# Optimization experiments

Measured on AMD Instinct MI355X. Metric: run time of the kernel, lower is better.

Reference implementation:

```python
import jax, jax.numpy as jnp
import numpy as np

D = 128
N_A = 50000
N_B = 50000
E = 600000
EPS = 1e-5

def setup_inputs() -> dict:
    key = jax.random.key(0)
    ks = jax.random.split(key, 16)
    s = 1.0 / np.sqrt(D)
    inp = {
        "x_A": jax.random.normal(ks[0], (N_A, D), jnp.float32),
        "x_B": jax.random.normal(ks[1], (N_B, D), jnp.float32),
        "ei_aa": jax.random.randint(ks[2], (2, E), 0, N_A),
        "ei_ba": jnp.stack([jax.random.randint(ks[3], (E,), 0, N_B),
                             jax.random.randint(ks[4], (E,), 0, N_A)]),
        "ei_ab": jnp.stack([jax.random.randint(ks[5], (E,), 0, N_A),
                             jax.random.randint(ks[6], (E,), 0, N_B)]),
        # SAGEConv params per edge type: W_l (neighbor), W_r (root), bias
        "W_l_aa": jax.random.uniform(ks[7], (D, D), jnp.float32, -s, s),
        "W_r_aa": jax.random.uniform(ks[8], (D, D), jnp.float32, -s, s),
        "b_aa": jnp.zeros((D,), jnp.float32),
        "W_l_ba": jax.random.uniform(ks[9], (D, D), jnp.float32, -s, s),
        "W_r_ba": jax.random.uniform(ks[10], (D, D), jnp.float32, -s, s),
        "b_ba": jnp.zeros((D,), jnp.float32),
        "W_l_ab": jax.random.uniform(ks[11], (D, D), jnp.float32, -s, s),
        "W_r_ab": jax.random.uniform(ks[12], (D, D), jnp.float32, -s, s),
        "b_ab": jnp.zeros((D,), jnp.float32),
        "gamma": jnp.ones((D,), jnp.float32),
        "beta": jnp.zeros((D,), jnp.float32),
    }
    return inp

def _sage(x_src, x_dst, ei, W_l, W_r, b, n_dst):
    # mean aggregation of gathered neighbor features (0 for isolated nodes, like PyG)
    msgs = x_src[ei[0]]                                            # [E, D]
    ssum = jax.ops.segment_sum(msgs, ei[1], num_segments=n_dst)    # [n_dst, D]
    cnt = jax.ops.segment_sum(jnp.ones((ei.shape[1], 1), x_src.dtype), ei[1], num_segments=n_dst)
    mean = ssum / jnp.maximum(cnt, 1.0)
    return mean @ W_l.T + x_dst @ W_r.T + b

def _layernorm(x, gamma, beta):
    mu = jnp.mean(x, axis=-1, keepdims=True)
    var = jnp.mean(jnp.square(x - mu), axis=-1, keepdims=True)
    return (x - mu) * jax.lax.rsqrt(var + EPS) * gamma + beta

def reference(x_A, x_B, ei_aa, ei_ba, ei_ab,
              W_l_aa, W_r_aa, b_aa, W_l_ba, W_r_ba, b_ba,
              W_l_ab, W_r_ab, b_ab, gamma, beta):
    # HeteroConv(aggr='sum'): sum conv outputs per destination node type
    out_A = (_sage(x_A, x_A, ei_aa, W_l_aa, W_r_aa, b_aa, N_A)
             + _sage(x_B, x_A, ei_ba, W_l_ba, W_r_ba, b_ba, N_A))
    out_B = _sage(x_A, x_B, ei_ab, W_l_ab, W_r_ab, b_ab, N_B)
    out_A = jax.nn.relu(_layernorm(out_A, gamma, beta))
    out_B = jax.nn.relu(_layernorm(out_B, gamma, beta))
    return out_A, out_B
```

## Files before the change

### kernel.cpp

```cpp
#include <hip/hip_runtime.h>

#define NNODE 50000
#define NEDGE 600000
#define NDST 150000
#define NEALL 1800000
#define BSZ 147
#define NBKT 1021
#define EPB 8192
#define P5B 220
#define PREPB 81
#define ECAP 3072

typedef __attribute__((ext_vector_type(8))) __bf16 bf16x8;
typedef __attribute__((ext_vector_type(4))) float f32x4;
typedef __attribute__((ext_vector_type(4))) unsigned int u32x4;

__device__ int dtype_of(const void* gamma) {
    unsigned int g = *(const unsigned int*)gamma;
    if (g == 0x3F803F80u) return 0;
    if (g == 0x3C003C00u) return 1;
    return 2;
}

__device__ float bf2f(unsigned short u) {
    unsigned int x = ((unsigned int)u) << 16;
    float f;
    __builtin_memcpy(&f, &x, 4);
    return f;
}

__device__ float bflo(unsigned int w) {
    unsigned int x = w << 16;
    float f;
    __builtin_memcpy(&f, &x, 4);
    return f;
}
__device__ float bfhi(unsigned int w) {
    unsigned int x = w & 0xFFFF0000u;
    float f;
    __builtin_memcpy(&f, &x, 4);
    return f;
}

__device__ unsigned short f2bf(float f) {
    unsigned int x;
    __builtin_memcpy(&x, &f, 4);
    unsigned int r = (x + 0x7FFFu + ((x >> 16) & 1u)) >> 16;
    return (unsigned short)r;
}

__device__ float ldf(const void* p, int i, int dt) {
    if (dt == 0) return bf2f(((const unsigned short*)p)[i]);
    if (dt == 1) return (float)(((const _Float16*)p)[i]);
    return ((const float*)p)[i];
}

__device__ void stf(void* p, int i, int dt, float v) {
    if (dt == 0) ((unsigned short*)p)[i] = f2bf(v);
    else if (dt == 1) ((_Float16*)p)[i] = (_Float16)v;
    else ((float*)p)[i] = v;
}

__device__ void edge4(const int* ei_aa, const int* ei_ba, const int* ei_ab,
                      int e, int4* d4, int4* s4) {
    const int* dbase;
    const int* sbase;
    int add;
    if (e < NEDGE) { sbase = ei_aa + e; dbase = ei_aa + NEDGE + e; add = 0; }
    else if (e < 2 * NEDGE) {
        int ee = e - NEDGE;
        sbase = ei_ba + ee; dbase = ei_ba + NEDGE + ee; add = 50000;
    } else {
        int ee = e - 2 * NEDGE;
        sbase = ei_ab + ee; dbase = ei_ab + NEDGE + ee; add = 100000;
    }
    int4 d = *(const int4*)dbase;
    d.x += add; d.y += add; d.z += add; d.w += add;
    *d4 = d;
    *s4 = *(const int4*)sbase;
}

__device__ void prep_body(int idx, const void* Wl_aa, const void* Wr_aa,
                          const void* b_aa, const void* Wl_ba, const void* Wr_ba,
                          const void* b_ba, const void* Wl_ab, const void* Wr_ab,
                          const void* b_ab, unsigned short* WA, unsigned short* WB,
                          float* biasA, float* biasB, int dt) {
    if (idx < 49152) {
        int n = idx / 384;
        int k = idx % 384;
        float v;
        if (k < 128) v = ldf(Wl_aa, n * 128 + k, dt);
        else if (k < 256) v = ldf(Wl_ba, n * 128 + k - 128, dt);
        else v = ldf(Wr_aa, n * 128 + k - 256, dt) + ldf(Wr_ba, n * 128 + k - 256, dt);
        WA[idx] = f2bf(v);
    } else if (idx < 49152 + 32768) {
        int i = idx - 49152;
        int n = i / 256;
        int k = i % 256;
        float v;
        if (k < 128) v = ldf(Wl_ab, n * 128 + k, dt);
        else v = ldf(Wr_ab, n * 128 + k - 128, dt);
        WB[i] = f2bf(v);
    } else if (idx < 49152 + 32768 + 128) {
        int j = idx - (49152 + 32768);
        biasA[j] = ldf(b_aa, j, dt) + ldf(b_ba, j, dt);
    } else if (idx < 49152 + 32768 + 256) {
        int j = idx - (49152 + 32768 + 128);
        biasB[j] = ldf(b_ab, j, dt);
    }
}

__global__ __launch_bounds__(1024) void p5_sort(
    const int* ei_aa, const int* ei_ba, const int* ei_ab,
    unsigned int* blkBuf, int* bbCnt, int* ibOfs,
    const void* Wl_aa, const void* Wr_aa, const void* b_aa,
    const void* Wl_ba, const void* Wr_ba, const void* b_ba,
    const void* Wl_ab, const void* Wr_ab, const void* b_ab,
    unsigned short* WA, unsigned short* WB,
    float* biasA, float* biasB, const void* gam) {
    int t = threadIdx.x;
    if (blockIdx.x >= P5B) {
        int dt = dtype_of(gam);
        int idx = (blockIdx.x - P5B) * 1024 + t;
        prep_body(idx, Wl_aa, Wr_aa, b_aa, Wl_ba, Wr_ba, b_ba,
                  Wl_ab, Wr_ab, b_ab, WA, WB, biasA, biasB, dt);
        return;
    }
    __shared__ int cnt[NBKT];
    __shared__ int ls[1024];
    __shared__ unsigned int buf[EPB];
    int4 dreg[2], sreg[2];
    bool val[2];
    int e0 = blockIdx.x * EPB + t * 8;
#pragma unroll
    for (int u = 0; u < 2; ++u) {
        int e = e0 + u * 4;
        val[u] = e < NEALL;
        if (val[u]) edge4(ei_aa, ei_ba, ei_ab, e, &dreg[u], &sreg[u]);
    }
    if (t < NBKT) cnt[t] = 0;
    __syncthreads();
#pragma unroll
    for (int u = 0; u < 2; ++u) {
        if (val[u]) {
            atomicAdd(&cnt[dreg[u].x / BSZ], 1);
            atomicAdd(&cnt[dreg[u].y / BSZ], 1);
            atomicAdd(&cnt[dreg[u].z / BSZ], 1);
            atomicAdd(&cnt[dreg[u].w / BSZ], 1);
        }
    }
    __syncthreads();
    int v = (t < NBKT) ? cnt[t] : 0;
    ls[t] = v;
    __syncthreads();
    for (int o = 1; o < 1024; o <<= 1) {
        int add = (t >= o) ? ls[t - o] : 0;
        __syncthreads();
        ls[t] += add;
        __syncthreads();
    }
    if (t < NBKT) {
        int excl = ls[t] - v;
        bbCnt[blockIdx.x * NBKT + t] = v;
        ibOfs[blockIdx.x * NBKT + t] = excl;
        cnt[t] = excl;
    }
    __syncthreads();
#pragma unroll
    for (int u = 0; u < 2; ++u) {
        if (val[u]) {
            int dv[4] = {dreg[u].x, dreg[u].y, dreg[u].z, dreg[u].w};
            int sv[4] = {sreg[u].x, sreg[u].y, sreg[u].z, sreg[u].w};
#pragma unroll
            for (int w = 0; w < 4; ++w) {
                int bkt = dv[w] / BSZ;
                int dl = dv[w] - bkt * BSZ;
                int r = atomicAdd(&cnt[bkt], 1);
                buf[r] = ((unsigned int)dl << 16) | (unsigned int)sv[w];
            }
        }
    }
    __syncthreads();
    unsigned int* dst = blkBuf + blockIdx.x * EPB;
#pragma unroll
    for (int u = 0; u < 2; ++u) {
        int idx = t * 8 + u * 4;
        __builtin_nontemporal_store(*(const u32x4*)&buf[idx], (u32x4*)&dst[idx]);
    }
}

__global__ __launch_bounds__(512, 8) void p6g_kernel(
    const unsigned int* blkBuf, const int* bbCnt, const int* ibOfs,
    const void* x_A, const void* x_B,
    unsigned short* mean1, unsigned short* mean2, unsigned short* mean3,
    const void* gam) {
    __shared__ int rp[256];
    __shared__ int runSrc[P5B];
    __shared__ unsigned int ebuf[ECAP];
    __shared__ unsigned short ebuf2[ECAP];
    __shared__ int rowLds[BSZ + 1];
    __shared__ int h[BSZ];
    __shared__ int cur[BSZ];
    __shared__ int sc[256];
    int t = threadIdx.x;
    int j = blockIdx.x;
    int dt = dtype_of(gam);
    int wave = t >> 6;
    int lane = t & 63;

    if (t < 256) {
        int c = (t < P5B) ? bbCnt[t * NBKT + j] : 0;
        rp[t] = c;
        if (t < P5B) runSrc[t] = t * EPB + ibOfs[t * NBKT + j];
    }
    __syncthreads();
    for (int o = 1; o < 256; o <<= 1) {
        int add = (t < 256 && t >= o) ? rp[t - o] : 0;
        __syncthreads();
        if (t < 256) rp[t] += add;
        __syncthreads();
    }
    int tot = rp[P5B - 1];
    bool staged = tot <= ECAP;

    if (staged) {
        for (int r = wave; r < P5B; r += 8) {
            int base = r ? rp[r - 1] : 0;
            int n = rp[r] - base;
            int gs = runSrc[r];
            for (int k = lane; k < n; k += 64)
                ebuf[base + k] = __builtin_nontemporal_load(&blkBuf[gs + k]);
        }
    }
    if (t < BSZ) h[t] = 0;
    __syncthreads();
    if (staged) {
        for (int i = t; i < tot; i += 512)
            atomicAdd(&h[(int)(ebuf[i] >> 16)], 1);
    } else {
        for (int r = wave; r < P5B; r += 8) {
            int base = r ? rp[r - 1] : 0;
            int n = rp[r] - base;
            int gs = runSrc[r];
            for (int k = lane; k < n; k += 64)
                atomicAdd(&h[(int)(blkBuf[gs + k] >> 16)], 1);
        }
    }
    __syncthreads();
    if (t < 256) sc[t] = (t < BSZ) ? h[t] : 0;
    __syncthreads();
    for (int o = 1; o < 256; o <<= 1) {
        int add = (t < 256 && t >= o) ? sc[t - o] : 0;
        __syncthreads();
        if (t < 256) sc[t] += add;
        __syncthreads();
    }
    if (t < BSZ) {
        int excl = sc[t] - h[t];
        rowLds[t] = excl;
        cur[t] = excl;
    }
    if (t == 0) rowLds[BSZ] = tot;
    __syncthreads();
    if (staged) {
        for (int i = t; i < tot; i += 512) {
            unsigned int w = ebuf[i];
            int pos = atomicAdd(&cur[(int)(w >> 16)], 1);
            ebuf2[pos] = (unsigned short)(w & 0xFFFFu);
        }
    }
    __syncthreads();

    int sub = lane >> 4;
    int col = lane & 15;
    for (int dl = wave; dl < BSZ; dl += 8) {
        int d = j * BSZ + dl;
        if (d >= NDST) break;
        const void* x;
        unsigned short* mean;
        int node;
        if (d < 50000) { x = x_A; mean = mean1; node = d; }
        else if (d < 100000) { x = x_B; mean = mean2; node = d - 50000; }
        else { x = x_A; mean = mean3; node = d - 100000; }

        if (!staged) {
            float b0 = 0.f, b1 = 0.f;
            int deg = 0;
            for (int r = 0; r < P5B; ++r) {
                int base = r ? rp[r - 1] : 0;
                int n = rp[r] - base;
                int gs = runSrc[r];
                for (int k = 0; k < n; ++k) {
                    unsigned int w = blkBuf[gs + k];
                    if ((int)(w >> 16) == dl) {
                        int src = (int)(w & 0xFFFFu);
                        if (dt == 0) {
                            unsigned int vv = ((const unsigned int*)x)[src * 64 + lane];
                            b0 += bflo(vv);
                            b1 += bfhi(vv);
                        } else {
                            b0 += ldf(x, src * 128 + 2 * lane, dt);
                            b1 += ldf(x, src * 128 + 2 * lane + 1, dt);
                        }
                        ++deg;
                    }
                }
            }
            float inv = deg ? 1.0f / (float)deg : 0.0f;
            ((unsigned int*)mean)[node * 64 + lane] =
                (unsigned int)f2bf(b0 * inv) | ((unsigned int)f2bf(b1 * inv) << 16);
            continue;
        }

        int beg = rowLds[dl];
        int end = rowLds[dl + 1];

        if (dt == 0) {
            const u32x4* xq = (const u32x4*)x;
            float a[8];
#pragma unroll
            for (int q = 0; q < 8; ++q) a[q] = 0.0f;
            for (int i = beg; i < end; i += 16) {
                int e0 = i + sub;
                int e1 = i + 4 + sub;
                int e2 = i + 8 + sub;
                int e3 = i + 12 + sub;
                bool p0 = e0 < end;
                bool p1 = e1 < end;
                bool p2 = e2 < end;
                bool p3 = e3 < end;
                int s0 = ebuf2[p0 ? e0 : beg];
                int s1 = ebuf2[p1 ? e1 : beg];
                int s2 = ebuf2[p2 ? e2 : beg];
                int s3 = ebuf2[p3 ? e3 : beg];
                u32x4 w0 = xq[s0 * 16 + col];
                u32x4 w1 = xq[s1 * 16 + col];
                u32x4 w2 = xq[s2 * 16 + col];
                u32x4 w3 = xq[s3 * 16 + col];
                if (!p0) w0 = u32x4{0u, 0u, 0u, 0u};
                if (!p1) w1 = u32x4{0u, 0u, 0u, 0u};
                if (!p2) w2 = u32x4{0u, 0u, 0u, 0u};
                if (!p3) w3 = u32x4{0u, 0u, 0u, 0u};
                a[0] += (bflo(w0.x) + bflo(w1.x)) + (bflo(w2.x) + bflo(w3.x));
                a[1] += (bfhi(w0.x) + bfhi(w1.x)) + (bfhi(w2.x) + bfhi(w3.x));
                a[2] += (bflo(w0.y) + bflo(w1.y)) + (bflo(w2.y) + bflo(w3.y));
                a[3] += (bfhi(w0.y) + bfhi(w1.y)) + (bfhi(w2.y) + bfhi(w3.y));
                a[4] += (bflo(w0.z) + bflo(w1.z)) + (bflo(w2.z) + bflo(w3.z));
                a[5] += (bfhi(w0.z) + bfhi(w1.z)) + (bfhi(w2.z) + bfhi(w3.z));
                a[6] += (bflo(w0.w) + bflo(w1.w)) + (bflo(w2.w) + bflo(w3.w));
                a[7] += (bfhi(w0.w) + bfhi(w1.w)) + (bfhi(w2.w) + bfhi(w3.w));
            }
#pragma unroll
            for (int q = 0; q < 8; ++q) {
                a[q] += __shfl_xor(a[q], 16);
                a[q] += __shfl_xor(a[q], 32);
            }
            float inv = (end > beg) ? 1.0f / (float)(end - beg) : 0.0f;
            if (lane < 16) {
                u32x4 o;
                o.x = (unsigned int)f2bf(a[0] * inv) | ((unsigned int)f2bf(a[1] * inv) << 16);
                o.y = (unsigned int)f2bf(a[2] * inv) | ((unsigned int)f2bf(a[3] * inv) << 16);
                o.z = (unsigned int)f2bf(a[4] * inv) | ((unsigned int)f2bf(a[5] * inv) << 16);
                o.w = (unsigned int)f2bf(a[6] * inv) | ((unsigned int)f2bf(a[7] * inv) << 16);
                __builtin_nontemporal_store(o, (u32x4*)mean + node * 16 + lane);
            }
        } else {
            float b0 = 0.f, b1 = 0.f;
            for (int i = beg; i < end; ++i) {
                int src = ebuf2[i];
                b0 += ldf(x, src * 128 + 2 * lane, dt);
                b1 += ldf(x, src * 128 + 2 * lane + 1, dt);
            }
            float inv = (end > beg) ? 1.0f / (float)(end - beg) : 0.0f;
            ((unsigned int*)mean)[node * 64 + lane] =
                (unsigned int)f2bf(b0 * inv) | ((unsigned int)f2bf(b1 * inv) << 16);
        }
    }
}

__device__ bf16x8 pack8(const float* f) {
    unsigned short u[8];
    for (int j = 0; j < 8; ++j) u[j] = f2bf(f[j]);
    bf16x8 r;
    __builtin_memcpy(&r, u, 16);
    return r;
}

template <int KTOT>
__device__ bf16x8 loadA(const unsigned short* mean1, const unsigned short* mean2,
                        const void* x, int r, int k, int dt) {
    if (k < 128) {
        return *(const bf16x8*)(mean1 + r * 128 + k);
    }
    if (KTOT == 384 && k < 256) {
        return *(const bf16x8*)(mean2 + r * 128 + (k - 128));
    }
    int kx = k - (KTOT - 128);
    if (dt == 0) {
        return *(const bf16x8*)((const unsigned short*)x + r * 128 + kx);
    }
    float f[8];
    for (int j = 0; j < 8; ++j) f[j] = ldf(x, r * 128 + kx + j, dt);
    return pack8(f);
}

template <int KTOT>
__device__ void gemm_body(int bx, const unsigned short* mean1,
                          const unsigned short* mean2, const void* x,
                          const unsigned short* Wu, const float* bias,
                          const void* gam, const void* bet, void* out,
                          int rowOff, int dt) {
    int lane = threadIdx.x & 63;
    int wave = threadIdx.x >> 6;
    int q16 = lane >> 4;
    int l16 = lane & 15;
    int mBase = (bx * 4 + wave) * 32;

    int r0 = mBase + l16;
    int r1 = mBase + 16 + l16;
    if (r0 > NNODE - 1) r0 = NNODE - 1;
    if (r1 > NNODE - 1) r1 = NNODE - 1;

    f32x4 acc[2][8];
    for (int rt = 0; rt < 2; ++rt)
        for (int tt = 0; tt < 8; ++tt) acc[rt][tt] = f32x4{0.f, 0.f, 0.f, 0.f};

    const int NCH = KTOT / 32;
    for (int ck = 0; ck < NCH; ++ck) {
        int k = ck * 32 + q16 * 8;
        bf16x8 a0 = loadA<KTOT>(mean1, mean2, x, r0, k, dt);
        bf16x8 a1 = loadA<KTOT>(mean1, mean2, x, r1, k, dt);
#pragma unroll
        for (int tt = 0; tt < 8; ++tt) {
            int n = tt * 16 + l16;
            bf16x8 b = *(const bf16x8*)(Wu + n * KTOT + k);
            acc[0][tt] = __builtin_amdgcn_mfma_f32_16x16x32_bf16(a0, b, acc[0][tt], 0, 0, 0);
            acc[1][tt] = __builtin_amdgcn_mfma_f32_16x16x32_bf16(a1, b, acc[1][tt], 0, 0, 0);
        }
    }

    float g[8], be[8], bs[8];
    for (int tt = 0; tt < 8; ++tt) {
        int j = tt * 16 + l16;
        g[tt] = ldf(gam, j, dt);
        be[tt] = ldf(bet, j, dt);
        bs[tt] = bias[j];
    }

    for (int rt = 0; rt < 2; ++rt) {
        for (int q = 0; q < 4; ++q) {
            int row = mBase + rt * 16 + q16 * 4 + q;
            float v[8];
            float s = 0.f, ss = 0.f;
            for (int tt = 0; tt < 8; ++tt) {
                v[tt] = acc[rt][tt][q] + bs[tt];
                s += v[tt];
                ss += v[tt] * v[tt];
            }
            for (int off = 1; off <= 8; off <<= 1) {
                s += __shfl_xor(s, off);
                ss += __shfl_xor(ss, off);
            }
            float m = s * (1.0f / 128.0f);
            float var = ss * (1.0f / 128.0f) - m * m;
            float rstd = rsqrtf(var + 1e-5f);
            if (row < NNODE) {
                for (int tt = 0; tt < 8; ++tt) {
                    float o = (v[tt] - m) * rstd * g[tt] + be[tt];
                    if (o < 0.0f) o = 0.0f;
                    stf(out, (rowOff + row) * 128 + tt * 16 + l16, dt, o);
                }
            }
        }
    }
}

__global__ __launch_bounds__(256) void gemm_ln_all(
    const unsigned short* mean1, const unsigned short* mean2,
    const unsigned short* mean3, const void* x_A, const void* x_B,
    const unsigned short* WA, const unsigned short* WB,
    const float* bA, const float* bB,
    const void* gam, const void* bet, void* out) {
    int dt = dtype_of(gam);
    if (blockIdx.x < 391)
        gemm_body<384>(blockIdx.x, mean1, mean2, x_A, WA, bA, gam, bet, out, 0, dt);
    else
        gemm_body<256>(blockIdx.x - 391, mean3, nullptr, x_B, WB, bB, gam, bet, out,
                       NNODE, dt);
}

extern "C" void kernel_launch(void* const* d_in, const int* in_sizes, int n_in,
                              void* d_out, int out_size, void* d_ws, size_t ws_size,
                              hipStream_t stream) {
    const void* x_A = d_in[0];
    const void* x_B = d_in[1];
    const int* ei_aa = (const int*)d_in[2];
    const int* ei_ba = (const int*)d_in[3];
    const int* ei_ab = (const int*)d_in[4];
    const void* W_l_aa = d_in[5];
    const void* W_r_aa = d_in[6];
    const void* b_aa = d_in[7];
    const void* W_l_ba = d_in[8];
    const void* W_r_ba = d_in[9];
    const void* b_ba = d_in[10];
    const void* W_l_ab = d_in[11];
    const void* W_r_ab = d_in[12];
    const void* b_ab = d_in[13];
    const void* gam = d_in[14];
    const void* bet = d_in[15];

    int* bbCnt = (int*)d_ws;
    int* ibOfs = bbCnt + P5B * NBKT;
    unsigned int* blkBuf = (unsigned int*)(ibOfs + P5B * NBKT);
    unsigned short* mean1 = (unsigned short*)(blkBuf + P5B * EPB);
    unsigned short* mean2 = mean1 + 6400000;
    unsigned short* mean3 = mean2 + 6400000;
    unsigned short* WA = mean3 + 6400000;
    unsigned short* WB = WA + 49152;
    float* bA = (float*)(WB + 32768);
    float* bB = bA + 128;

    p5_sort<<<P5B + PREPB, 1024, 0, stream>>>(
        ei_aa, ei_ba, ei_ab, blkBuf, bbCnt, ibOfs,
        W_l_aa, W_r_aa, b_aa, W_l_ba, W_r_ba, b_ba,
        W_l_ab, W_r_ab, b_ab, WA, WB, bA, bB, gam);

    p6g_kernel<<<NBKT, 512, 0, stream>>>(blkBuf, bbCnt, ibOfs, x_A, x_B,
                                         mean1, mean2, mean3, gam);

    gemm_ln_all<<<782, 256, 0, stream>>>(mean1, mean2, mean3, x_A, x_B,
                                         WA, WB, bA, bB, gam, bet, d_out);
}
```

Before: 370.9 us.

## Fuse mean aggregation with GEMM+LayerNorm, keeping means in swizzled LDS

Merges the aggregation kernel and the GEMM+LayerNorm kernel into one. Buckets now hold 48 A-nodes, with both of their incoming edge types interleaved, or 96 B-nodes, so each block can compute the full output rows for its nodes. The bf16 means are written to XOR-swizzled shared memory instead of three global mean buffers, which removes a global write/read round trip and a kernel launch. In exchange each block runs the GEMM with only 8 waves and reads weights per block from global/L2. It also adds LDS atomics for the row statistics and cuts the staged edge capacity, so more buckets may fall onto the slow unstaged path.

Result: slower. 537.4 us (+44.9%).

```diff
diff --git a/kernel.cpp b/kernel.cpp
--- a/kernel.cpp
+++ b/kernel.cpp
@@ -4,12 +4,12 @@
 #define NEDGE 600000
 #define NDST 150000
 #define NEALL 1800000
-#define BSZ 147
-#define NBKT 1021
+#define ABKT 1042
+#define NBKT 1563
 #define EPB 8192
 #define P5B 220
 #define PREPB 81
-#define ECAP 3072
+#define ECAP 2048
 
 typedef __attribute__((ext_vector_type(8))) __bf16 bf16x8;
 typedef __attribute__((ext_vector_type(4))) float f32x4;
@@ -59,6 +59,24 @@
     if (dt == 0) ((unsigned short*)p)[i] = f2bf(v);
     else if (dt == 1) ((_Float16*)p)[i] = (_Float16)v;
     else ((float*)p)[i] = v;
+}
+
+__device__ int2 bucket_of(int d) {
+    int2 r;
+    if (d < 50000) {
+        r.x = d / 48;
+        r.y = (d - r.x * 48) * 2;
+    } else if (d < 100000) {
+        int n = d - 50000;
+        r.x = n / 48;
+        r.y = (n - r.x * 48) * 2 + 1;
+    } else {
+        int n = d - 100000;
+        int j = n / 96;
+        r.x = ABKT + j;
+        r.y = n - j * 96;
+    }
+    return r;
 }
 
 __device__ void edge4(const int* ei_aa, const int* ei_ba, const int* ei_ab,
@@ -139,19 +157,23 @@
         if (val[u]) edge4(ei_aa, ei_ba, ei_ab, e, &dreg[u], &sreg[u]);
     }
     if (t < NBKT) cnt[t] = 0;
+    if (t + 1024 < NBKT) cnt[t + 1024] = 0;
     __syncthreads();
 #pragma unroll
     for (int u = 0; u < 2; ++u) {
         if (val[u]) {
-            atomicAdd(&cnt[dreg[u].x / BSZ], 1);
-            atomicAdd(&cnt[dreg[u].y / BSZ], 1);
-            atomicAdd(&cnt[dreg[u].z / BSZ], 1);
-            atomicAdd(&cnt[dreg[u].w / BSZ], 1);
-        }
-    }
-    __syncthreads();
-    int v = (t < NBKT) ? cnt[t] : 0;
-    ls[t] = v;
+            atomicAdd(&cnt[bucket_of(dreg[u].x).x], 1);
+            atomicAdd(&cnt[bucket_of(dreg[u].y).x], 1);
+            atomicAdd(&cnt[bucket_of(dreg[u].z).x], 1);
+            atomicAdd(&cnt[bucket_of(dreg[u].w).x], 1);
+        }
+    }
+    __syncthreads();
+    int b0 = 2 * t, b1 = 2 * t + 1;
+    int v0 = (b0 < NBKT) ? cnt[b0] : 0;
+    int v1 = (b1 < NBKT) ? cnt[b1] : 0;
+    int s = v0 + v1;
+    ls[t] = s;
     __syncthreads();
     for (int o = 1; o < 1024; o <<= 1) {
         int add = (t >= o) ? ls[t - o] : 0;
@@ -159,12 +181,17 @@
         ls[t] += add;
         __syncthreads();
     }
-    if (t < NBKT) {
-        int excl = ls[t] - v;
-        bbCnt[blockIdx.x * NBKT + t] = v;
-        ibOfs[blockIdx.x * NBKT + t] = excl;
-        cnt[t] = excl;
-    }
+    int base = ls[t] - s;
+    if (b0 < NBKT) {
+        bbCnt[blockIdx.x * NBKT + b0] = v0;
+        ibOfs[blockIdx.x * NBKT + b0] = base;
+    }
+    if (b1 < NBKT) {
+        bbCnt[blockIdx.x * NBKT + b1] = v1;
+        ibOfs[blockIdx.x * NBKT + b1] = base + v0;
+    }
+    if (b0 < NBKT) cnt[b0] = base;
+    if (b1 < NBKT) cnt[b1] = base + v0;
     __syncthreads();
 #pragma unroll
     for (int u = 0; u < 2; ++u) {
@@ -173,10 +200,9 @@
             int sv[4] = {sreg[u].x, sreg[u].y, sreg[u].z, sreg[u].w};
 #pragma unroll
             for (int w = 0; w < 4; ++w) {
-                int bkt = dv[w] / BSZ;
-                int dl = dv[w] - bkt * BSZ;
-                int r = atomicAdd(&cnt[bkt], 1);
-                buf[r] = ((unsigned int)dl << 16) | (unsigned int)sv[w];
+                int2 b = bucket_of(dv[w]);
+                int r = atomicAdd(&cnt[b.x], 1);
+                buf[r] = ((unsigned int)b.y << 16) | (unsigned int)sv[w];
             }
         }
     }
@@ -189,30 +215,141 @@
     }
 }
 
-__global__ __launch_bounds__(512, 8) void p6g_kernel(
+__device__ bf16x8 lds_readA(const unsigned short* meanLds, int dl, int kbyte) {
+    int key = (dl ^ (dl >> 1)) & 7;
+    int byte = dl * 256 + (kbyte ^ (key << 4));
+    return *(const bf16x8*)((const char*)meanLds + byte);
+}
+
+__device__ bf16x8 pack8(const float* f) {
+    unsigned short u[8];
+    for (int j = 0; j < 8; ++j) u[j] = f2bf(f[j]);
+    bf16x8 r;
+    __builtin_memcpy(&r, u, 16);
+    return r;
+}
+
+__device__ bf16x8 x_read(const void* x, int row, int kx, int dt) {
+    if (row > NNODE - 1) row = NNODE - 1;
+    if (dt == 0) return *(const bf16x8*)((const unsigned short*)x + row * 128 + kx);
+    float f[8];
+    for (int j = 0; j < 8; ++j) f[j] = ldf(x, row * 128 + kx + j, dt);
+    return pack8(f);
+}
+
+template <int KTOT, int NRT>
+__device__ void gemm_phase(int tIdx, int n0, const unsigned short* meanLds,
+                           const void* x, const unsigned short* Wu,
+                           const float* bias, const void* gam, const void* bet,
+                           void* out, int rowOff, int dt,
+                           float* sums, float* sumsq) {
+    int lane = tIdx & 63;
+    int wave = tIdx >> 6;
+    int q16 = lane >> 4;
+    int l16 = lane & 15;
+    int col = wave * 16 + l16;
+    float g = ldf(gam, col, dt);
+    float be_ = ldf(bet, col, dt);
+    float bs = bias[col];
+    const int NCH = KTOT / 32;
+
+    for (int g0 = 0; g0 < NRT; g0 += 3) {
+        f32x4 acc[3];
+#pragma unroll
+        for (int rt = 0; rt < 3; ++rt) acc[rt] = f32x4{0.f, 0.f, 0.f, 0.f};
+        for (int ck = 0; ck < NCH; ++ck) {
+            int k = ck * 32 + q16 * 8;
+            bf16x8 b = *(const bf16x8*)(Wu + col * KTOT + k);
+#pragma unroll
+            for (int rt = 0; rt < 3; ++rt) {
+                int r = (g0 + rt) * 16 + l16;
+                bf16x8 a;
+                if (KTOT == 384) {
+                    if (k < 128) a = lds_readA(meanLds, 2 * r, k * 2);
+                    else if (k < 256) a = lds_readA(meanLds, 2 * r + 1, (k - 128) * 2);
+                    else a = x_read(x, n0 + r, k - 256, dt);
+                } else {
+                    if (k < 128) a = lds_readA(meanLds, r, k * 2);
+                    else a = x_read(x, n0 + r, k - 128, dt);
+                }
+                acc[rt] = __builtin_amdgcn_mfma_f32_16x16x32_bf16(a, b, acc[rt], 0, 0, 0);
+            }
+        }
+#pragma unroll
+        for (int rt = 0; rt < 3; ++rt) {
+            for (int q = 0; q < 4; ++q) {
+                float v = acc[rt][q] + bs;
+                float s = v, ss = v * v;
+                for (int off = 1; off <= 8; off <<= 1) {
+                    s += __shfl_xor(s, off);
+                    ss += __shfl_xor(ss, off);
+                }
+                if (l16 == 0) {
+                    int row = (g0 + rt) * 16 + q16 * 4 + q;
+                    atomicAdd(&sums[row], s);
+                    atomicAdd(&sumsq[row], ss);
+                }
+            }
+        }
+        __syncthreads();
+        if (tIdx < 48) {
+            int row = g0 * 16 + tIdx;
+            float s = sums[row], ss = sumsq[row];
+            float m = s * (1.0f / 128.0f);
+            float var = ss * (1.0f / 128.0f) - m * m;
+            sums[row] = m;
+            sumsq[row] = rsqrtf(var + 1e-5f);
+        }
+        __syncthreads();
+#pragma unroll
+        for (int rt = 0; rt < 3; ++rt) {
+            for (int q = 0; q < 4; ++q) {
+                int row = (g0 + rt) * 16 + q16 * 4 + q;
+                int node = n0 + row;
+                if (node < NNODE) {
+                    float m = sums[row];
+                    float rstd = sumsq[row];
+                    float o = (acc[rt][q] + bs - m) * rstd * g + be_;
+                    if (o < 0.0f) o = 0.0f;
+                    stf(out, (rowOff + node) * 128 + col, dt, o);
+                }
+            }
+        }
+    }
+}
+
+__global__ __launch_bounds__(512, 8) void pg_kernel(
     const unsigned int* blkBuf, const int* bbCnt, const int* ibOfs,
     const void* x_A, const void* x_B,
-    unsigned short* mean1, unsigned short* mean2, unsigned short* mean3,
-    const void* gam) {
+    const unsigned short* WA, const unsigned short* WB,
+    const float* bA, const float* bB,
+    const void* gam, const void* bet, void* out) {
     __shared__ int rp[256];
     __shared__ int runSrc[P5B];
-    __shared__ unsigned int ebuf[ECAP];
+    __shared__ unsigned int uShared[6144];
     __shared__ unsigned short ebuf2[ECAP];
-    __shared__ int rowLds[BSZ + 1];
-    __shared__ int h[BSZ];
-    __shared__ int cur[BSZ];
+    __shared__ int rowLds[97];
+    __shared__ int h[96];
+    __shared__ int cur[96];
     __shared__ int sc[256];
+    __shared__ float sums[96];
+    __shared__ float sumsq[96];
+    unsigned int* ebuf = uShared;
+    unsigned short* meanLds = (unsigned short*)uShared;
+
     int t = threadIdx.x;
     int j = blockIdx.x;
     int dt = dtype_of(gam);
     int wave = t >> 6;
     int lane = t & 63;
+    bool isA = j < ABKT;
 
     if (t < 256) {
         int c = (t < P5B) ? bbCnt[t * NBKT + j] : 0;
         rp[t] = c;
         if (t < P5B) runSrc[t] = t * EPB + ibOfs[t * NBKT + j];
     }
+    if (t < 96) { sums[t] = 0.f; sumsq[t] = 0.f; }
     __syncthreads();
     for (int o = 1; o < 256; o <<= 1) {
         int add = (t < 256 && t >= o) ? rp[t - o] : 0;
@@ -232,7 +369,7 @@
                 ebuf[base + k] = __builtin_nontemporal_load(&blkBuf[gs + k]);
         }
     }
-    if (t < BSZ) h[t] = 0;
+    if (t < 96) h[t] = 0;
     __syncthreads();
     if (staged) {
         for (int i = t; i < tot; i += 512)
@@ -247,7 +384,7 @@
         }
     }
     __syncthreads();
-    if (t < 256) sc[t] = (t < BSZ) ? h[t] : 0;
+    if (t < 256) sc[t] = (t < 96) ? h[t] : 0;
     __syncthreads();
     for (int o = 1; o < 256; o <<= 1) {
         int add = (t < 256 && t >= o) ? sc[t - o] : 0;
@@ -255,12 +392,12 @@
         if (t < 256) sc[t] += add;
         __syncthreads();
     }
-    if (t < BSZ) {
+    if (t < 96) {
         int excl = sc[t] - h[t];
         rowLds[t] = excl;
         cur[t] = excl;
     }
-    if (t == 0) rowLds[BSZ] = tot;
+    if (t == 0) rowLds[96] = tot;
     __syncthreads();
     if (staged) {
         for (int i = t; i < tot; i += 512) {
@@ -272,16 +409,19 @@
     __syncthreads();
 
     int sub = lane >> 4;
-    int col = lane & 15;
-    for (int dl = wave; dl < BSZ; dl += 8) {
-        int d = j * BSZ + dl;
-        if (d >= NDST) break;
+    int col16 = lane & 15;
+    for (int dl = wave; dl < 96; dl += 8) {
+        int node;
         const void* x;
-        unsigned short* mean;
-        int node;
-        if (d < 50000) { x = x_A; mean = mean1; node = d; }
-        else if (d < 100000) { x = x_B; mean = mean2; node = d - 50000; }
-        else { x = x_A; mean = mean3; node = d - 100000; }
+        if (isA) {
+            node = j * 48 + (dl >> 1);
+            x = (dl & 1) ? x_B : x_A;
+        } else {
+            node = (j - ABKT) * 96 + dl;
+            x = x_A;
+        }
+        if (node >= NNODE) continue;
+        int key = (dl ^ (dl >> 1)) & 7;
 
         if (!staged) {
             float b0 = 0.f, b1 = 0.f;
@@ -307,7 +447,8 @@
                 }
             }
             float inv = deg ? 1.0f / (float)deg : 0.0f;
-            ((unsigned int*)mean)[node * 64 + lane] =
+            int byte = dl * 256 + ((lane * 4) ^ (key << 4));
+            *(unsigned int*)((char*)meanLds + byte) =
                 (unsigned int)f2bf(b0 * inv) | ((unsigned int)f2bf(b1 * inv) << 16);
             continue;
         }
@@ -333,10 +474,10 @@
                 int s1 = ebuf2[p1 ? e1 : beg];
                 int s2 = ebuf2[p2 ? e2 : beg];
                 int s3 = ebuf2[p3 ? e3 : beg];
-                u32x4 w0 = xq[s0 * 16 + col];
-                u32x4 w1 = xq[s1 * 16 + col];
-                u32x4 w2 = xq[s2 * 16 + col];
-                u32x4 w3 = xq[s3 * 16 + col];
+                u32x4 w0 = xq[s0 * 16 + col16];
+                u32x4 w1 = xq[s1 * 16 + col16];
+                u32x4 w2 = xq[s2 * 16 + col16];
+                u32x4 w3 = xq[s3 * 16 + col16];
                 if (!p0) w0 = u32x4{0u, 0u, 0u, 0u};
                 if (!p1) w1 = u32x4{0u, 0u, 0u, 0u};
                 if (!p2) w2 = u32x4{0u, 0u, 0u, 0u};
@@ -362,7 +503,8 @@
                 o.y = (unsigned int)f2bf(a[2] * inv) | ((unsigned int)f2bf(a[3] * inv) << 16);
                 o.z = (unsigned int)f2bf(a[4] * inv) | ((unsigned int)f2bf(a[5] * inv) << 16);
                 o.w = (unsigned int)f2bf(a[6] * inv) | ((unsigned int)f2bf(a[7] * inv) << 16);
-                __builtin_nontemporal_store(o, (u32x4*)mean + node * 16 + lane);
+                int byte = dl * 256 + ((lane * 16) ^ (key << 4));
+                *(u32x4*)((char*)meanLds + byte) = o;
             }
         } else {
             float b0 = 0.f, b1 = 0.f;
@@ -372,121 +514,19 @@
                 b1 += ldf(x, src * 128 + 2 * lane + 1, dt);
             }
             float inv = (end > beg) ? 1.0f / (float)(end - beg) : 0.0f;
-            ((unsigned int*)mean)[node * 64 + lane] =
+            int byte = dl * 256 + ((lane * 4) ^ (key << 4));
+            *(unsigned int*)((char*)meanLds + byte) =
                 (unsigned int)f2bf(b0 * inv) | ((unsigned int)f2bf(b1 * inv) << 16);
         }
     }
-}
-
-__device__ bf16x8 pack8(const float* f) {
-    unsigned short u[8];
-    for (int j = 0; j < 8; ++j) u[j] = f2bf(f[j]);
-    bf16x8 r;
-    __builtin_memcpy(&r, u, 16);
-    return r;
-}
-
-template <int KTOT>
-__device__ bf16x8 loadA(const unsigned short* mean1, const unsigned short* mean2,
-                        const void* x, int r, int k, int dt) {
-    if (k < 128) {
-        return *(const bf16x8*)(mean1 + r * 128 + k);
-    }
-    if (KTOT == 384 && k < 256) {
-        return *(const bf16x8*)(mean2 + r * 128 + (k - 128));
-    }
-    int kx = k - (KTOT - 128);
-    if (dt == 0) {
-        return *(const bf16x8*)((const unsigned short*)x + r * 128 + kx);
-    }
-    float f[8];
-    for (int j = 0; j < 8; ++j) f[j] = ldf(x, r * 128 + kx + j, dt);
-    return pack8(f);
-}
-
-template <int KTOT>
-__device__ void gemm_body(int bx, const unsigned short* mean1,
-                          const unsigned short* mean2, const void* x,
-                          const unsigned short* Wu, const float* bias,
-                          const void* gam, const void* bet, void* out,
-                          int rowOff, int dt) {
-    int lane = threadIdx.x & 63;
-    int wave = threadIdx.x >> 6;
-    int q16 = lane >> 4;
-    int l16 = lane & 15;
-    int mBase = (bx * 4 + wave) * 32;
-
-    int r0 = mBase + l16;
-    int r1 = mBase + 16 + l16;
-    if (r0 > NNODE - 1) r0 = NNODE - 1;
-    if (r1 > NNODE - 1) r1 = NNODE - 1;
-
-    f32x4 acc[2][8];
-    for (int rt = 0; rt < 2; ++rt)
-        for (int tt = 0; tt < 8; ++tt) acc[rt][tt] = f32x4{0.f, 0.f, 0.f, 0.f};
-
-    const int NCH = KTOT / 32;
-    for (int ck = 0; ck < NCH; ++ck) {
-        int k = ck * 32 + q16 * 8;
-        bf16x8 a0 = loadA<KTOT>(mean1, mean2, x, r0, k, dt);
-        bf16x8 a1 = loadA<KTOT>(mean1, mean2, x, r1, k, dt);
-#pragma unroll
-        for (int tt = 0; tt < 8; ++tt) {
-            int n = tt * 16 + l16;
-            bf16x8 b = *(const bf16x8*)(Wu + n * KTOT + k);
-            acc[0][tt] = __builtin_amdgcn_mfma_f32_16x16x32_bf16(a0, b, acc[0][tt], 0, 0, 0);
-            acc[1][tt] = __builtin_amdgcn_mfma_f32_16x16x32_bf16(a1, b, acc[1][tt], 0, 0, 0);
-        }
-    }
-
-    float g[8], be[8], bs[8];
-    for (int tt = 0; tt < 8; ++tt) {
-        int j = tt * 16 + l16;
-        g[tt] = ldf(gam, j, dt);
-        be[tt] = ldf(bet, j, dt);
-        bs[tt] = bias[j];
-    }
-
-    for (int rt = 0; rt < 2; ++rt) {
-        for (int q = 0; q < 4; ++q) {
-            int row = mBase + rt * 16 + q16 * 4 + q;
-            float v[8];
-            float s = 0.f, ss = 0.f;
-            for (int tt = 0; tt < 8; ++tt) {
-                v[tt] = acc[rt][tt][q] + bs[tt];
-                s += v[tt];
-                ss += v[tt] * v[tt];
-            }
-            for (int off = 1; off <= 8; off <<= 1) {
-                s += __shfl_xor(s, off);
-                ss += __shfl_xor(ss, off);
-            }
-            float m = s * (1.0f / 128.0f);
-            float var = ss * (1.0f / 128.0f) - m * m;
-            float rstd = rsqrtf(var + 1e-5f);
-            if (row < NNODE) {
-                for (int tt = 0; tt < 8; ++tt) {
-                    float o = (v[tt] - m) * rstd * g[tt] + be[tt];
-                    if (o < 0.0f) o = 0.0f;
-                    stf(out, (rowOff + row) * 128 + tt * 16 + l16, dt, o);
-                }
-            }
-        }
-    }
-}
-
-__global__ __launch_bounds__(256) void gemm_ln_all(
-    const unsigned short* mean1, const unsigned short* mean2,
-    const unsigned short* mean3, const void* x_A, const void* x_B,
-    const unsigned short* WA, const unsigned short* WB,
-    const float* bA, const float* bB,
-    const void* gam, const void* bet, void* out) {
-    int dt = dtype_of(gam);
-    if (blockIdx.x < 391)
-        gemm_body<384>(blockIdx.x, mean1, mean2, x_A, WA, bA, gam, bet, out, 0, dt);
+    __syncthreads();
+
+    if (isA)
+        gemm_phase<384, 3>(t, j * 48, meanLds, x_A, WA, bA, gam, bet, out,
+                           0, dt, sums, sumsq);
     else
-        gemm_body<256>(blockIdx.x - 391, mean3, nullptr, x_B, WB, bB, gam, bet, out,
-                       NNODE, dt);
+        gemm_phase<256, 6>(t, (j - ABKT) * 96, meanLds, x_B, WB, bB, gam, bet, out,
+                           NNODE, dt, sums, sumsq);
 }
 
 extern "C" void kernel_launch(void* const* d_in, const int* in_sizes, int n_in,
@@ -512,10 +552,7 @@
     int* bbCnt = (int*)d_ws;
     int* ibOfs = bbCnt + P5B * NBKT;
     unsigned int* blkBuf = (unsigned int*)(ibOfs + P5B * NBKT);
-    unsigned short* mean1 = (unsigned short*)(blkBuf + P5B * EPB);
-    unsigned short* mean2 = mean1 + 6400000;
-    unsigned short* mean3 = mean2 + 6400000;
-    unsigned short* WA = mean3 + 6400000;
+    unsigned short* WA = (unsigned short*)(blkBuf + P5B * EPB);
     unsigned short* WB = WA + 49152;
     float* bA = (float*)(WB + 32768);
     float* bB = bA + 128;
@@ -525,9 +562,6 @@
         W_l_aa, W_r_aa, b_aa, W_l_ba, W_r_ba, b_ba,
         W_l_ab, W_r_ab, b_ab, WA, WB, bA, bB, gam);
 
-    p6g_kernel<<<NBKT, 512, 0, stream>>>(blkBuf, bbCnt, ibOfs, x_A, x_B,
-                                         mean1, mean2, mean3, gam);
-
-    gemm_ln_all<<<782, 256, 0, stream>>>(mean1, mean2, mean3, x_A, x_B,
-                                         WA, WB, bA, bB, gam, bet, d_out);
-}
+    pg_kernel<<<NBKT, 512, 0, stream>>>(blkBuf, bbCnt, ibOfs, x_A, x_B,
+                                        WA, WB, bA, bB, gam, bet, d_out);
+}
```
